# Performance work log

Hardware: AMD Instinct MI355X
Metric: run time of the kernel (lower is better)

## Reference

```python
import jax, jax.numpy as jnp
import numpy as np

K = 1.0          # curvature of all manifolds
EPS = 1e-6
LN_EPS = 1e-5    # torch LayerNorm eps
POWER_K = 3.0

N_NODES, N_EDGES, IN_DIM, HID, HEADS = 50000, 250000, 128, 32, 4


def _time(s):
    # Lorentz time coordinate from space part
    return jnp.sqrt(jnp.sum(s * s, axis=-1, keepdims=True) + K)


def _hyp_point(s):
    return jnp.concatenate([_time(s), s], axis=-1)


def _layernorm(s, g, b):
    m = jnp.mean(s, axis=-1, keepdims=True)
    v = jnp.var(s, axis=-1, keepdims=True)
    return (s - m) / jnp.sqrt(v + LN_EPS) * g + b


def _fp(x, p=POWER_K):
    # ||x||_2 / ||x^p||_2 * x^p  (TransConv.fp)
    nx = jnp.sqrt(jnp.sum(x * x, axis=-1, keepdims=True))
    xp = x ** p
    nxp = jnp.sqrt(jnp.sum(xp * xp, axis=-1, keepdims=True))
    return nx / nxp * xp


def setup_inputs() -> dict:
    key = jax.random.key(0)
    ks = jax.random.split(key, 12)
    f32 = jnp.float32
    inp = {
        'h': jax.random.normal(ks[0], (N_NODES, IN_DIM), f32),
        'src': jax.random.randint(ks[1], (N_EDGES,), 0, N_NODES, jnp.int32),
        'dst': jax.random.randint(ks[2], (N_EDGES,), 0, N_NODES, jnp.int32),
        # fcs[0][0]: HypLinear(in_dim -> hidden), euclidean input (+1 time col)
        'W_fc': (jax.random.normal(ks[3], (IN_DIM + 1, HID), f32) / np.float32(np.sqrt(IN_DIM + 1))),
        'b_fc': jnp.zeros((HID,), f32),
        # bns[0]: HypLayerNorm(hidden)
        'ln1_g': jnp.ones((HID,), f32), 'ln1_b': jnp.zeros((HID,), f32),
        # Wq/Wk/Wv: per-head HypLinear(hidden -> hidden), input is (hidden+1)-dim point
        'Wq': jax.random.normal(ks[4], (HEADS, HID + 1, HID), f32) / np.float32(np.sqrt(HID + 1)),
        'bq': jnp.zeros((HEADS, HID), f32),
        'Wk': jax.random.normal(ks[5], (HEADS, HID + 1, HID), f32) / np.float32(np.sqrt(HID + 1)),
        'bk': jnp.zeros((HEADS, HID), f32),
        'Wv': jax.random.normal(ks[6], (HEADS, HID + 1, HID), f32) / np.float32(np.sqrt(HID + 1)),
        'bv': jnp.zeros((HEADS, HID), f32),
        # hidden_to_out[0]: HypLinear(hidden -> hidden)
        'W_ho': jax.random.normal(ks[7], (HID + 1, HID), f32) / np.float32(np.sqrt(HID + 1)),
        'b_ho': jnp.zeros((HID,), f32),
        # final HypLayerNorm (self.bn)
        'ln2_g': jnp.ones((HID,), f32), 'ln2_b': jnp.zeros((HID,), f32),
        'norm_scale': jnp.ones((), f32),
    }
    return inp


def reference(h, src, dst, W_fc, b_fc, ln1_g, ln1_b, Wq, bq, Wk, bk, Wv, bv,
              W_ho, b_ho, ln2_g, ln2_b, norm_scale):
    N = h.shape[0]
    # iter == 0: lift euclidean features, prepend ones for time column
    x1 = jnp.concatenate([jnp.ones_like(h[..., :1]), h], axis=-1)  # [N, IN+1]
    hyp = _hyp_point(x1 @ W_fc + b_fc)                             # [N, HID+1]
    residual = hyp
    # HypLayerNorm -> HypActivation(leaky_relu) -> HypDropout (eval: identity).
    # Intermediate time coords are recomputed/discarded; only the final point's
    # full (HID+1) coords feed the q/k/v HypLinears.
    s = jax.nn.leaky_relu(_layernorm(hyp[..., 1:], ln1_g, ln1_b))
    node = _hyp_point(s)                                           # [N, HID+1]
    # per-head HypLinear; edge_attention only uses the space part [:, :, 1:],
    # so the q/k/v time coords are never consumed and are omitted here.
    q = jnp.einsum('nt,htd->nhd', node, Wq) + bq                   # [N, H, HID]
    k = jnp.einsum('nt,htd->nhd', node, Wk) + bk
    v = jnp.einsum('nt,htd->nhd', node, Wv) + bv
    # gather to edges
    qe = q[dst]                                                    # [E, H, HID]
    ke = k[src]
    ve = v[src]
    inv_scale = 1.0 / jnp.abs(norm_scale)
    phi_q = _fp((jax.nn.leaky_relu(qe) + EPS) * inv_scale)
    phi_k = _fp((jax.nn.leaky_relu(ke) + EPS) * inv_scale)
    phi_v = (jax.nn.leaky_relu(ve) + EPS) * inv_scale
    # global (over all edges) kernelized linear attention moments
    ktv = jnp.einsum('ehm,ehd->hmd', phi_k, phi_v)                 # [H, HID, HID]
    numerator = jnp.einsum('ehm,hmd->ehd', phi_q, ktv)             # [E, H, HID]
    denominator = jnp.einsum('ehd,hd->eh', phi_q, jnp.sum(phi_k, axis=0))[..., None]
    attn = jnp.mean(numerator / (denominator + EPS), axis=1)       # [E, HID]
    t = jnp.sqrt(jnp.sum(attn * attn, axis=-1, keepdims=True) + K)
    edge_in = jnp.concatenate([t, attn], axis=-1)                  # [E, HID+1]
    edge_out = _hyp_point(edge_in @ W_ho + b_ho)                   # [E, HID+1]
    # fn.copy_e + fn.mean over incoming edges per destination node
    seg_sum = jax.ops.segment_sum(edge_out, dst, num_segments=N)
    cnt = jax.ops.segment_sum(jnp.ones((edge_out.shape[0], 1), edge_out.dtype), dst, num_segments=N)
    agg = jnp.where(cnt > 0, seg_sum / jnp.maximum(cnt, 1.0), 0.0)
    # Lorentz mid_point of (agg, residual)
    ave = 0.5 * (agg + residual)
    inner = -ave[..., :1] ** 2 + jnp.sum(ave[..., 1:] ** 2, axis=-1, keepdims=True)
    denom = jnp.sqrt(jnp.maximum(jnp.abs(inner), EPS))
    hnew = jnp.sqrt(K) * ave / denom
    # final HypLayerNorm + HypDropout(eval)
    out = _hyp_point(_layernorm(hnew[..., 1:], ln2_g, ln2_b))
    return out
```

## Files before the change

kernel.cpp:

```cpp
#include <hip/hip_runtime.h>

#define NN 50000
#define NE 250000
#define KTVC 4224
#define NBX 512

__device__ __forceinline__ float lrelu(float x) { return x > 0.f ? x : 0.01f * x; }

__global__ __launch_bounds__(256) void k_zero(int* __restrict__ p) {
    int i = blockIdx.x * 256 + threadIdx.x;
    if (i < 100000) p[i] = 0;
}

__global__ __launch_bounds__(256) void k_hist(const int* __restrict__ src,
                                              const int* __restrict__ dst,
                                              int* __restrict__ cnt_src,
                                              int* __restrict__ cnt_dst) {
    int e = blockIdx.x * 256 + threadIdx.x;
    if (e < NE) {
        atomicAdd(&cnt_src[src[e]], 1);
        atomicAdd(&cnt_dst[dst[e]], 1);
    }
}

__global__ __launch_bounds__(512) void k_fc(const float* __restrict__ h,
                                            const float* __restrict__ Wfc,
                                            const float* __restrict__ bfc,
                                            const float* __restrict__ g1,
                                            const float* __restrict__ b1,
                                            float* __restrict__ resid,
                                            float* __restrict__ node33T) {
    __shared__ float hch[128][33];
    __shared__ float stat_t[8][128];
    __shared__ float stat2_t[4][128];
    const int tid = threadIdx.x;
    const int q = __builtin_amdgcn_readfirstlane((threadIdx.x >> 7) & 3);
    const int nl = tid & 127;
    const int base = blockIdx.x * 128;
    const int n = base + nl;

    float acc[8];
#pragma unroll
    for (int jj = 0; jj < 8; ++jj) acc[jj] = Wfc[q * 8 + jj] + bfc[q * 8 + jj];

    for (int c = 0; c < 4; ++c) {
        __syncthreads();
#pragma unroll
        for (int r = 0; r < 8; ++r) {
            int idx = r * 512 + tid;
            int sn = idx >> 5, t = idx & 31;
            int gn = base + sn;
            hch[sn][t] = h[(size_t)((gn < NN) ? gn : 0) * 128 + c * 32 + t];
        }
        __syncthreads();
        for (int i = 0; i < 32; ++i) {
            float hv = hch[nl][i];
            const float* wr = Wfc + (size_t)(1 + c * 32 + i) * 32 + q * 8;
#pragma unroll
            for (int jj = 0; jj < 8; ++jj) acc[jj] = fmaf(hv, wr[jj], acc[jj]);
        }
    }
    float ps = 0.f, pq2 = 0.f;
#pragma unroll
    for (int jj = 0; jj < 8; ++jj) { ps += acc[jj]; pq2 += acc[jj] * acc[jj]; }
    stat_t[q * 2 + 0][nl] = ps;
    stat_t[q * 2 + 1][nl] = pq2;
    __syncthreads();
    float sm = stat_t[0][nl] + stat_t[2][nl] + stat_t[4][nl] + stat_t[6][nl];
    float sq = stat_t[1][nl] + stat_t[3][nl] + stat_t[5][nl] + stat_t[7][nl];
    float mean = sm * (1.f / 32.f);
    float var = fmaxf(sq * (1.f / 32.f) - mean * mean, 0.f);
    float rstd = rsqrtf(var + 1e-5f);
    float lr[8];
    float pl2 = 0.f;
#pragma unroll
    for (int jj = 0; jj < 8; ++jj) {
        int j = q * 8 + jj;
        float ln = (acc[jj] - mean) * rstd * g1[j] + b1[j];
        lr[jj] = lrelu(ln);
        pl2 += lr[jj] * lr[jj];
    }
    stat2_t[q][nl] = pl2;
    __syncthreads();
    float l2 = stat2_t[0][nl] + stat2_t[1][nl] + stat2_t[2][nl] + stat2_t[3][nl];
    if (n < NN) {
        float* rrow = resid + (size_t)n * 36;
#pragma unroll
        for (int jj = 0; jj < 8; ++jj) rrow[1 + q * 8 + jj] = acc[jj];
#pragma unroll
        for (int jj = 0; jj < 8; ++jj) node33T[(size_t)(1 + q * 8 + jj) * NN + n] = lr[jj];
        if (q == 0) {
            rrow[0] = sqrtf(sq + 1.f);
            node33T[n] = sqrtf(l2 + 1.f);
        }
    }
}

__global__ __launch_bounds__(128) void k_qkv(const float* __restrict__ node33T,
                                             const float* __restrict__ Wk, const float* __restrict__ bk,
                                             const float* __restrict__ Wv, const float* __restrict__ bv,
                                             const float* __restrict__ nscale,
                                             const int* __restrict__ cnt_src,
                                             float* __restrict__ partial) {
    __shared__ float nlds[64][33];
    __shared__ float pk[64][36];
    __shared__ float pv[64][36];
    const int tid = threadIdx.x;
    const int w_u = __builtin_amdgcn_readfirstlane(tid >> 6);
    const int h_u = __builtin_amdgcn_readfirstlane(blockIdx.y);
    const int lane = tid & 63;
    const float inv = 1.f / fabsf(nscale[0]);
    const float* W = ((w_u == 0) ? Wk : Wv) + (size_t)h_u * 33 * 32;
    const float* bb = ((w_u == 0) ? bk : bv) + h_u * 32;
    const int mm4 = lane >> 3, d4 = lane & 7;

    float facc[16];
#pragma unroll
    for (int t = 0; t < 16; ++t) facc[t] = 0.f;
    float ks[4] = {0.f, 0.f, 0.f, 0.f};

    const int ntiles = (NN + 63) / 64;
    for (int tile = blockIdx.x; tile < ntiles; tile += NBX) {
        const int base = tile * 64;
        const int n = base + lane;
        for (int idx = tid; idx < 2112; idx += 128) {
            int c = idx >> 6, sn = idx & 63;
            int gn = base + sn;
            nlds[sn][c] = node33T[(size_t)c * NN + ((gn < NN) ? gn : 0)];
        }
        __syncthreads();

        float acc[32];
#pragma unroll
        for (int j = 0; j < 32; ++j) acc[j] = bb[j];
        for (int i = 0; i < 33; ++i) {
            float hv = nlds[lane][i];
            const float* wr = W + (size_t)i * 32;
#pragma unroll
            for (int j = 0; j < 32; ++j) acc[j] = fmaf(hv, wr[j], acc[j]);
        }

        if (w_u == 0) {
            const float wc = (n < NN) ? (float)cnt_src[n] : 0.f;
            float s2 = 0.f, s6 = 0.f;
#pragma unroll
            for (int j = 0; j < 32; ++j) {
                float x = (lrelu(acc[j]) + 1e-6f) * inv;
                s2 += x * x;
                float x3 = x * x * x;
                s6 += x3 * x3;
                acc[j] = x3;
            }
            const float factor = sqrtf(s2) / sqrtf(s6) * wc;
#pragma unroll
            for (int j = 0; j < 32; ++j) pk[lane][j] = factor * acc[j];
        } else {
#pragma unroll
            for (int j = 0; j < 32; ++j) pv[lane][j] = (lrelu(acc[j]) + 1e-6f) * inv;
        }
        __syncthreads();

#pragma unroll 4
        for (int n0 = 0; n0 < 32; ++n0) {
            const int nn = w_u * 32 + n0;
            float4 pkv = *(const float4*)&pk[nn][mm4 * 4];
            float4 pvv = *(const float4*)&pv[nn][d4 * 4];
            float pkv_a[4] = {pkv.x, pkv.y, pkv.z, pkv.w};
            float pvv_a[4] = {pvv.x, pvv.y, pvv.z, pvv.w};
#pragma unroll
            for (int i = 0; i < 4; ++i)
#pragma unroll
                for (int jj = 0; jj < 4; ++jj)
                    facc[i * 4 + jj] = fmaf(pkv_a[i], pvv_a[jj], facc[i * 4 + jj]);
            if (d4 == 0) {
#pragma unroll
                for (int i = 0; i < 4; ++i) ks[i] += pkv_a[i];
            }
        }
        __syncthreads();
    }

    float* scr = &pk[0][0];
    float* scr2 = &pv[0][0];
    if (w_u == 0) {
#pragma unroll
        for (int t = 0; t < 16; ++t) scr[lane * 16 + t] = facc[t];
        if (d4 == 0) {
#pragma unroll
            for (int i = 0; i < 4; ++i) scr2[mm4 * 4 + i] = ks[i];
        }
    }
    __syncthreads();
    if (w_u == 1) {
        float* pb = partial + (size_t)blockIdx.x * KTVC + h_u * 1056;
#pragma unroll
        for (int i = 0; i < 4; ++i)
#pragma unroll
            for (int jj = 0; jj < 4; ++jj)
                pb[(mm4 * 4 + i) * 32 + d4 * 4 + jj] =
                    facc[i * 4 + jj] + scr[lane * 16 + i * 4 + jj];
        if (d4 == 0) {
#pragma unroll
            for (int i = 0; i < 4; ++i)
                pb[1024 + mm4 * 4 + i] = ks[i] + scr2[mm4 * 4 + i];
        }
    }
}

__global__ __launch_bounds__(256) void k_red(const float* __restrict__ partial,
                                             float* __restrict__ ktvf) {
    __shared__ float red[8][33];
    const int tid = threadIdx.x;
    const int col = tid & 31, g = tid >> 5;
    const int c = blockIdx.x * 32 + col;
    float s = 0.f;
    for (int r = g * 64; r < (g + 1) * 64; ++r)
        s += partial[(size_t)r * KTVC + c];
    red[g][col] = s;
    __syncthreads();
    if (tid < 32) {
        float t0 = (red[0][tid] + red[1][tid]) + (red[2][tid] + red[3][tid]);
        float t1 = (red[4][tid] + red[5][tid]) + (red[6][tid] + red[7][tid]);
        ktvf[blockIdx.x * 32 + tid] = t0 + t1;
    }
}

__global__ __launch_bounds__(256) void k_final(const float* __restrict__ node33T,
                                               const float* __restrict__ Wq, const float* __restrict__ bq,
                                               const float* __restrict__ nscale,
                                               const float* __restrict__ ktvf,
                                               const float* __restrict__ Who,
                                               const float* __restrict__ bho,
                                               const float* __restrict__ g2,
                                               const float* __restrict__ b2,
                                               const int* __restrict__ cnt_dst,
                                               const float* __restrict__ resid,
                                               float* __restrict__ out) {
    __shared__ float nlds[64][37];
    __shared__ float att[4][64][33];
    __shared__ float who_lds[33 * 32];
    __shared__ float g2l[32], b2l[32], bhol[32];
    const int tid = threadIdx.x;
    const int h_u = __builtin_amdgcn_readfirstlane(tid >> 6);
    const int lane = tid & 63;
    const int base = blockIdx.x * 64;
    const float inv = 1.f / fabsf(nscale[0]);

#pragma unroll
    for (int r = 0; r < 9; ++r) {
        int idx = r * 256 + tid;
        if (idx < 2112) {
            int c = idx >> 6, sn = idx & 63;
            int gn = base + sn;
            nlds[sn][c] = node33T[(size_t)c * NN + ((gn < NN) ? gn : 0)];
        }
    }
    for (int f = tid; f < 33 * 32; f += 256) who_lds[f] = Who[f];
    if (tid < 32) { g2l[tid] = g2[tid]; b2l[tid] = b2[tid]; bhol[tid] = bho[tid]; }
    __syncthreads();

    {
        float acc[32];
#pragma unroll
        for (int j = 0; j < 32; ++j) acc[j] = bq[h_u * 32 + j];
        const float* W = Wq + (size_t)h_u * 33 * 32;
        for (int i = 0; i < 33; ++i) {
            float hv = nlds[lane][i];
            const float* wr = W + (size_t)i * 32;
#pragma unroll
            for (int j = 0; j < 32; ++j) acc[j] = fmaf(hv, wr[j], acc[j]);
        }
        float s2 = 0.f, s6 = 0.f;
#pragma unroll
        for (int j = 0; j < 32; ++j) {
            float x = (lrelu(acc[j]) + 1e-6f) * inv;
            s2 += x * x;
            float x3 = x * x * x;
            s6 += x3 * x3;
            acc[j] = x3;
        }
        const float factor = sqrtf(s2) / sqrtf(s6);
        const float* ksum = ktvf + h_u * 1056 + 1024;
        float den = 0.f;
#pragma unroll
        for (int j = 0; j < 32; ++j) { acc[j] *= factor; den += acc[j] * ksum[j]; }
        const float rd = 0.25f / (den + 1e-6f);
        float num[32];
#pragma unroll
        for (int d = 0; d < 32; ++d) num[d] = 0.f;
        const float* kt = ktvf + h_u * 1056;
#pragma unroll 2
        for (int t = 0; t < 32; ++t) {
            const float f = acc[t];
            const float* kr = kt + t * 32;
#pragma unroll
            for (int d = 0; d < 32; ++d) num[d] = fmaf(f, kr[d], num[d]);
        }
#pragma unroll
        for (int d = 0; d < 32; ++d) att[h_u][lane][d] = num[d] * rd;
    }
    __syncthreads();

    const int nl2 = tid >> 2, jq = tid & 3;
    const int n2 = base + nl2;
    const int nc = (n2 < NN) ? n2 : NN - 1;
    float attn[32];
#pragma unroll
    for (int d = 0; d < 32; ++d)
        attn[d] = ((att[0][nl2][d] + att[1][nl2][d]) + (att[2][nl2][d] + att[3][nl2][d]));
    float a2 = 0.f;
#pragma unroll
    for (int d = 0; d < 32; ++d) a2 += attn[d] * attn[d];
    const float tc = sqrtf(a2 + 1.f);
    float eo[8];
#pragma unroll
    for (int jj = 0; jj < 8; ++jj) {
        int j = jq * 8 + jj;
        eo[jj] = bhol[j] + tc * who_lds[j];
    }
#pragma unroll
    for (int d = 0; d < 32; ++d) {
        const float f = attn[d];
        const float* wr = &who_lds[(1 + d) * 32 + jq * 8];
#pragma unroll
        for (int jj = 0; jj < 8; ++jj) eo[jj] = fmaf(f, wr[jj], eo[jj]);
    }
    float e2 = 0.f;
#pragma unroll
    for (int jj = 0; jj < 8; ++jj) e2 += eo[jj] * eo[jj];
    e2 += __shfl_xor(e2, 1);
    e2 += __shfl_xor(e2, 2);
    const float te = sqrtf(e2 + 1.f);
    const float sc = (cnt_dst[nc] > 0) ? 1.f : 0.f;
    const float* rr = resid + (size_t)nc * 36;
    const float av0 = 0.5f * (sc * te + rr[0]);
    float avs[8];
    float pinner = 0.f;
#pragma unroll
    for (int jj = 0; jj < 8; ++jj) {
        avs[jj] = 0.5f * (sc * eo[jj] + rr[1 + jq * 8 + jj]);
        pinner += avs[jj] * avs[jj];
    }
    pinner += __shfl_xor(pinner, 1);
    pinner += __shfl_xor(pinner, 2);
    const float inner = pinner - av0 * av0;
    const float rdn = 1.f / sqrtf(fmaxf(fabsf(inner), 1e-6f));
    float pm = 0.f;
#pragma unroll
    for (int jj = 0; jj < 8; ++jj) { avs[jj] *= rdn; pm += avs[jj]; }
    pm += __shfl_xor(pm, 1);
    pm += __shfl_xor(pm, 2);
    const float mean = pm * (1.f / 32.f);
    float pv2 = 0.f;
#pragma unroll
    for (int jj = 0; jj < 8; ++jj) { float dd = avs[jj] - mean; pv2 += dd * dd; }
    pv2 += __shfl_xor(pv2, 1);
    pv2 += __shfl_xor(pv2, 2);
    const float rstd = rsqrtf(pv2 * (1.f / 32.f) + 1e-5f);
    float ln[8];
    float pl2 = 0.f;
#pragma unroll
    for (int jj = 0; jj < 8; ++jj) {
        int j = jq * 8 + jj;
        ln[jj] = (avs[jj] - mean) * rstd * g2l[j] + b2l[j];
        pl2 += ln[jj] * ln[jj];
    }
    pl2 += __shfl_xor(pl2, 1);
    pl2 += __shfl_xor(pl2, 2);
    if (n2 < NN) {
        float* orow = out + (size_t)n2 * 33;
#pragma unroll
        for (int jj = 0; jj < 8; ++jj) orow[1 + jq * 8 + jj] = ln[jj];
        if (jq == 0) orow[0] = sqrtf(pl2 + 1.f);
    }
}

extern "C" void kernel_launch(void* const* d_in, const int* in_sizes, int n_in,
                              void* d_out, int out_size, void* d_ws, size_t ws_size,
                              hipStream_t stream) {
    const float* h   = (const float*)d_in[0];
    const int* src   = (const int*)d_in[1];
    const int* dst   = (const int*)d_in[2];
    const float* Wfc = (const float*)d_in[3];
    const float* bfc = (const float*)d_in[4];
    const float* g1  = (const float*)d_in[5];
    const float* b1  = (const float*)d_in[6];
    const float* Wq  = (const float*)d_in[7];
    const float* bq  = (const float*)d_in[8];
    const float* Wk  = (const float*)d_in[9];
    const float* bk  = (const float*)d_in[10];
    const float* Wv  = (const float*)d_in[11];
    const float* bv  = (const float*)d_in[12];
    const float* Who = (const float*)d_in[13];
    const float* bho = (const float*)d_in[14];
    const float* g2  = (const float*)d_in[15];
    const float* b2  = (const float*)d_in[16];
    const float* nsc = (const float*)d_in[17];
    float* out = (float*)d_out;
    char* ws = (char*)d_ws;

    int* cnt_src   = (int*)(ws + 0);
    int* cnt_dst   = (int*)(ws + 200000);
    float* resid   = (float*)(ws + 400000);
    float* node33T = (float*)(ws + 7600000);
    float* part    = (float*)(ws + 14200000);
    float* ktvf    = (float*)(ws + 22852608);

    hipLaunchKernelGGL(k_zero, dim3(391), dim3(256), 0, stream, (int*)ws);
    hipLaunchKernelGGL(k_hist, dim3((NE + 255) / 256), dim3(256), 0, stream,
                       src, dst, cnt_src, cnt_dst);
    hipLaunchKernelGGL(k_fc, dim3((NN + 127) / 128), dim3(512), 0, stream,
                       h, Wfc, bfc, g1, b1, resid, node33T);
    hipLaunchKernelGGL(k_qkv, dim3(NBX, 4), dim3(128), 0, stream,
                       node33T, Wk, bk, Wv, bv, nsc, cnt_src, part);
    hipLaunchKernelGGL(k_red, dim3(KTVC / 32), dim3(256), 0, stream,
                       part, ktvf);
    hipLaunchKernelGGL(k_final, dim3((NN + 63) / 64), dim3(256), 0, stream,
                       node33T, Wq, bq, nsc, ktvf, Who, bho, g2, b2, cnt_dst, resid, out);
}
```

Baseline: 127.6 us.

## Restructure K/V projection with register-resident weights and per-column thread mapping

k_qkv now assigns one output column per lane, keeps that column of Wk and Wv in registers, and computes both K and V for 8 nodes per 32-lane group from LDS-staged node rows. Per-node norms for the power feature map are reduced with cross-lane shuffles. Each block now covers 128 nodes in a fixed 391-block grid with 256 threads instead of grid-striding 64-node tiles. The outer-product accumulation keeps a full 32-wide row per lane, and the per-group partials are merged in LDS. This is meant to remove the repeated global weight reads and the split K/V waves, at the cost of higher register pressure (66 weight plus 32 accumulator registers). k_red is adjusted to the new partial count.

```diff
diff --git a/kernel.cpp b/kernel.cpp
--- a/kernel.cpp
+++ b/kernel.cpp
@@ -3,7 +3,7 @@
 #define NN 50000
 #define NE 250000
 #define KTVC 4224
-#define NBX 512
+#define QBX 391
 
 __device__ __forceinline__ float lrelu(float x) { return x > 0.f ? x : 0.01f * x; }
 
@@ -96,114 +96,122 @@
     }
 }
 
-__global__ __launch_bounds__(128) void k_qkv(const float* __restrict__ node33T,
+__global__ __launch_bounds__(256) void k_qkv(const float* __restrict__ node33T,
                                              const float* __restrict__ Wk, const float* __restrict__ bk,
                                              const float* __restrict__ Wv, const float* __restrict__ bv,
                                              const float* __restrict__ nscale,
                                              const int* __restrict__ cnt_src,
                                              float* __restrict__ partial) {
-    __shared__ float nlds[64][33];
-    __shared__ float pk[64][36];
-    __shared__ float pv[64][36];
+    __shared__ float smem[7392];
+    float* nlds = smem;
+    float* ldsv = smem + 2304;
     const int tid = threadIdx.x;
-    const int w_u = __builtin_amdgcn_readfirstlane(tid >> 6);
-    const int h_u = __builtin_amdgcn_readfirstlane(blockIdx.y);
-    const int lane = tid & 63;
+    const int j = tid & 31;
+    const int g = tid >> 5;
+    const int h = blockIdx.y;
+    const int bb = blockIdx.x * 128;
     const float inv = 1.f / fabsf(nscale[0]);
-    const float* W = ((w_u == 0) ? Wk : Wv) + (size_t)h_u * 33 * 32;
-    const float* bb = ((w_u == 0) ? bk : bv) + h_u * 32;
-    const int mm4 = lane >> 3, d4 = lane & 7;
-
-    float facc[16];
-#pragma unroll
-    for (int t = 0; t < 16; ++t) facc[t] = 0.f;
-    float ks[4] = {0.f, 0.f, 0.f, 0.f};
-
-    const int ntiles = (NN + 63) / 64;
-    for (int tile = blockIdx.x; tile < ntiles; tile += NBX) {
-        const int base = tile * 64;
-        const int n = base + lane;
-        for (int idx = tid; idx < 2112; idx += 128) {
+
+    float wk[33], wv[33];
+#pragma unroll
+    for (int i = 0; i < 33; ++i) wk[i] = Wk[(size_t)(h * 33 + i) * 32 + j];
+#pragma unroll
+    for (int i = 0; i < 33; ++i) wv[i] = Wv[(size_t)(h * 33 + i) * 32 + j];
+    const float bbk = bk[h * 32 + j];
+    const float bbv = bv[h * 32 + j];
+
+    float facc[32];
+#pragma unroll
+    for (int d = 0; d < 32; ++d) facc[d] = 0.f;
+    float ksum = 0.f;
+
+    for (int s = 0; s < 2; ++s) {
+        __syncthreads();
+        for (int idx = tid; idx < 2112; idx += 256) {
             int c = idx >> 6, sn = idx & 63;
-            int gn = base + sn;
-            nlds[sn][c] = node33T[(size_t)c * NN + ((gn < NN) ? gn : 0)];
+            int gn = bb + s * 64 + sn;
+            nlds[sn * 36 + c] = node33T[(size_t)c * NN + ((gn < NN) ? gn : 0)];
         }
         __syncthreads();
 
-        float acc[32];
-#pragma unroll
-        for (int j = 0; j < 32; ++j) acc[j] = bb[j];
-        for (int i = 0; i < 33; ++i) {
-            float hv = nlds[lane][i];
-            const float* wr = W + (size_t)i * 32;
-#pragma unroll
-            for (int j = 0; j < 32; ++j) acc[j] = fmaf(hv, wr[j], acc[j]);
-        }
-
-        if (w_u == 0) {
-            const float wc = (n < NN) ? (float)cnt_src[n] : 0.f;
-            float s2 = 0.f, s6 = 0.f;
-#pragma unroll
-            for (int j = 0; j < 32; ++j) {
-                float x = (lrelu(acc[j]) + 1e-6f) * inv;
-                s2 += x * x;
-                float x3 = x * x * x;
-                s6 += x3 * x3;
-                acc[j] = x3;
+        float ack[8], acv[8];
+#pragma unroll
+        for (int nn = 0; nn < 8; ++nn) { ack[nn] = bbk; acv[nn] = bbv; }
+#pragma unroll
+        for (int nn = 0; nn < 8; ++nn) {
+            const float* row = &nlds[(g * 8 + nn) * 36];
+#pragma unroll
+            for (int i4 = 0; i4 < 8; ++i4) {
+                float4 hv = *(const float4*)&row[i4 * 4];
+                ack[nn] = fmaf(hv.x, wk[i4 * 4 + 0], ack[nn]);
+                acv[nn] = fmaf(hv.x, wv[i4 * 4 + 0], acv[nn]);
+                ack[nn] = fmaf(hv.y, wk[i4 * 4 + 1], ack[nn]);
+                acv[nn] = fmaf(hv.y, wv[i4 * 4 + 1], acv[nn]);
+                ack[nn] = fmaf(hv.z, wk[i4 * 4 + 2], ack[nn]);
+                acv[nn] = fmaf(hv.z, wv[i4 * 4 + 2], acv[nn]);
+                ack[nn] = fmaf(hv.w, wk[i4 * 4 + 3], ack[nn]);
+                acv[nn] = fmaf(hv.w, wv[i4 * 4 + 3], acv[nn]);
             }
-            const float factor = sqrtf(s2) / sqrtf(s6) * wc;
-#pragma unroll
-            for (int j = 0; j < 32; ++j) pk[lane][j] = factor * acc[j];
-        } else {
-#pragma unroll
-            for (int j = 0; j < 32; ++j) pv[lane][j] = (lrelu(acc[j]) + 1e-6f) * inv;
-        }
-        __syncthreads();
-
-#pragma unroll 4
-        for (int n0 = 0; n0 < 32; ++n0) {
-            const int nn = w_u * 32 + n0;
-            float4 pkv = *(const float4*)&pk[nn][mm4 * 4];
-            float4 pvv = *(const float4*)&pv[nn][d4 * 4];
-            float pkv_a[4] = {pkv.x, pkv.y, pkv.z, pkv.w};
-            float pvv_a[4] = {pvv.x, pvv.y, pvv.z, pvv.w};
-#pragma unroll
-            for (int i = 0; i < 4; ++i)
-#pragma unroll
-                for (int jj = 0; jj < 4; ++jj)
-                    facc[i * 4 + jj] = fmaf(pkv_a[i], pvv_a[jj], facc[i * 4 + jj]);
-            if (d4 == 0) {
-#pragma unroll
-                for (int i = 0; i < 4; ++i) ks[i] += pkv_a[i];
+            float hv32 = row[32];
+            ack[nn] = fmaf(hv32, wk[32], ack[nn]);
+            acv[nn] = fmaf(hv32, wv[32], acv[nn]);
+        }
+
+        float pk[8];
+#pragma unroll
+        for (int nn = 0; nn < 8; ++nn) {
+            const int gn = bb + s * 64 + g * 8 + nn;
+            float xk = (lrelu(ack[nn]) + 1e-6f) * inv;
+            float s2 = xk * xk;
+            float x3 = xk * xk * xk;
+            float s6 = x3 * x3;
+#pragma unroll
+            for (int msk = 16; msk >= 1; msk >>= 1) {
+                s2 += __shfl_xor(s2, msk);
+                s6 += __shfl_xor(s6, msk);
             }
-        }
-        __syncthreads();
-    }
-
-    float* scr = &pk[0][0];
-    float* scr2 = &pv[0][0];
-    if (w_u == 0) {
-#pragma unroll
-        for (int t = 0; t < 16; ++t) scr[lane * 16 + t] = facc[t];
-        if (d4 == 0) {
-#pragma unroll
-            for (int i = 0; i < 4; ++i) scr2[mm4 * 4 + i] = ks[i];
-        }
-    }
-    __syncthreads();
-    if (w_u == 1) {
-        float* pb = partial + (size_t)blockIdx.x * KTVC + h_u * 1056;
-#pragma unroll
-        for (int i = 0; i < 4; ++i)
-#pragma unroll
-            for (int jj = 0; jj < 4; ++jj)
-                pb[(mm4 * 4 + i) * 32 + d4 * 4 + jj] =
-                    facc[i * 4 + jj] + scr[lane * 16 + i * 4 + jj];
-        if (d4 == 0) {
-#pragma unroll
-            for (int i = 0; i < 4; ++i)
-                pb[1024 + mm4 * 4 + i] = ks[i] + scr2[mm4 * 4 + i];
-        }
+            const float wc = (gn < NN) ? (float)cnt_src[gn] : 0.f;
+            pk[nn] = sqrtf(s2) / sqrtf(s6) * wc * x3;
+            ksum += pk[nn];
+            float xv = (lrelu(acv[nn]) + 1e-6f) * inv;
+            ldsv[(g * 8 + nn) * 32 + j] = xv;
+        }
+
+#pragma unroll
+        for (int nn = 0; nn < 8; ++nn) {
+            const float* vr = &ldsv[(g * 8 + nn) * 32];
+            const float p = pk[nn];
+#pragma unroll
+            for (int d4 = 0; d4 < 8; ++d4) {
+                float4 vv = *(const float4*)&vr[d4 * 4];
+                facc[d4 * 4 + 0] = fmaf(p, vv.x, facc[d4 * 4 + 0]);
+                facc[d4 * 4 + 1] = fmaf(p, vv.y, facc[d4 * 4 + 1]);
+                facc[d4 * 4 + 2] = fmaf(p, vv.z, facc[d4 * 4 + 2]);
+                facc[d4 * 4 + 3] = fmaf(p, vv.w, facc[d4 * 4 + 3]);
+            }
+        }
+    }
+
+    __syncthreads();
+    if (g > 0) {
+        float* mg = &smem[(g - 1) * 1056 + j * 33];
+#pragma unroll
+        for (int d = 0; d < 32; ++d) mg[d] = facc[d];
+        mg[32] = ksum;
+    }
+    __syncthreads();
+    if (g == 0) {
+#pragma unroll
+        for (int ss = 0; ss < 7; ++ss) {
+            const float* mg = &smem[ss * 1056 + j * 33];
+#pragma unroll
+            for (int d = 0; d < 32; ++d) facc[d] += mg[d];
+            ksum += mg[32];
+        }
+        float* pb = partial + (size_t)blockIdx.x * KTVC + h * 1056;
+#pragma unroll
+        for (int d = 0; d < 32; ++d) pb[j * 32 + d] = facc[d];
+        pb[1024 + j] = ksum;
     }
 }
 
@@ -213,8 +221,9 @@
     const int tid = threadIdx.x;
     const int col = tid & 31, g = tid >> 5;
     const int c = blockIdx.x * 32 + col;
+    const int r0 = g * 49, r1 = min(r0 + 49, QBX);
     float s = 0.f;
-    for (int r = g * 64; r < (g + 1) * 64; ++r)
+    for (int r = r0; r < r1; ++r)
         s += partial[(size_t)r * KTVC + c];
     red[g][col] = s;
     __syncthreads();
@@ -411,7 +420,7 @@
                        src, dst, cnt_src, cnt_dst);
     hipLaunchKernelGGL(k_fc, dim3((NN + 127) / 128), dim3(512), 0, stream,
                        h, Wfc, bfc, g1, b1, resid, node33T);
-    hipLaunchKernelGGL(k_qkv, dim3(NBX, 4), dim3(128), 0, stream,
+    hipLaunchKernelGGL(k_qkv, dim3(QBX, 4), dim3(256), 0, stream,
                        node33T, Wk, bk, Wv, bv, nsc, cnt_src, part);
     hipLaunchKernelGGL(k_red, dim3(KTVC / 32), dim3(256), 0, stream,
                        part, ktvf);
```

Result: slower. 242.6 us (+90.0%).
